# Performance work log

Measured on AMD Instinct MI355X. Metric: run time of the kernel, lower is better.

## Reference

```python
import jax, jax.numpy as jnp
import numpy as np

B, S, F = 32, 8, 4
N0, N1, N2 = 2048, 4096, 2048
H, OUT = 1024, 256
IN = N0 + N1 + N2  # 8192
SC_LAYERS = 2


def setup_inputs() -> dict:
    key = jax.random.key(0)
    ks = jax.random.split(key, 16)
    rn = jax.random.normal
    inp = {
        'xs0': rn(ks[0], (B, S, N0), jnp.float32),
        'xs1': rn(ks[1], (B, S, N1), jnp.float32),
        'xs2': rn(ks[2], (B, S, N2), jnp.float32),
        # dense Laplacians, scaled so L@x keeps unit-ish variance
        'L0': rn(ks[3], (N0, N0), jnp.float32) / np.sqrt(N0).astype(np.float32),
        'L1': rn(ks[4], (N1, N1), jnp.float32) / np.sqrt(N1).astype(np.float32),
        'L2': rn(ks[5], (N2, N2), jnp.float32) / np.sqrt(N2).astype(np.float32),
        # per-layer, per-filter diagonal weights (std=0.01 as in torch init)
        'Wc0': 0.01 * rn(ks[6], (SC_LAYERS, F, N0), jnp.float32),
        'Wc1': 0.01 * rn(ks[7], (SC_LAYERS, F, N1), jnp.float32),
        'Wc2': 0.01 * rn(ks[8], (SC_LAYERS, F, N2), jnp.float32),
        # MLP params (xavier-ish)
        'W_in': rn(ks[9], (IN, H), jnp.float32) / np.sqrt(IN).astype(np.float32),
        'b_in': jnp.zeros((H,), jnp.float32),
        'W_h': rn(ks[10], (H, H), jnp.float32) / np.sqrt(H).astype(np.float32),
        'b_h': jnp.zeros((H,), jnp.float32),
        'W_out': rn(ks[11], (H, OUT), jnp.float32) / np.sqrt(H).astype(np.float32),
        'b_out': jnp.zeros((OUT,), jnp.float32),
    }
    return inp


def _conv_stack(x, L, Wc):
    # x: [B, S, n]; L: [n, n]; Wc: [layers, F, n]
    for l in range(Wc.shape[0]):
        # batched Laplacian matmul: (L @ x_bs) for every (b, s)
        Lx = jnp.einsum('bsn,mn->bsm', x, L)  # [B, S, n]
        # diagonal filter scaling + activation + sum over filters (fused)
        x = jax.nn.relu(Lx[:, :, None, :] * Wc[l][None, None, :, :]).sum(axis=2)
    return x


def reference(xs0, xs1, xs2, L0, L1, L2, Wc0, Wc1, Wc2,
              W_in, b_in, W_h, b_h, W_out, b_out):
    h = jnp.concatenate([
        _conv_stack(xs0, L0, Wc0),
        _conv_stack(xs1, L1, Wc1),
        _conv_stack(xs2, L2, Wc2),
    ], axis=-1)                      # [B, S, IN]
    h = h.sum(axis=1)                # sum over sequence -> [B, IN]
    h = jax.nn.relu(h @ W_in + b_in)
    h = jax.nn.relu(h @ W_h + b_h)   # single hidden layer (nn_layers=2)
    return h @ W_out + b_out         # [B, OUT]
```

## Files before the change

kernel.cpp:

```cpp
#include <hip/hip_runtime.h>
#include <hip/hip_bf16.h>


#define B_    32
#define S_    8
#define BS_   256
#define F_    4
#define IN_   8192
#define H_    1024
#define OUT_  256

#define L_TOT  25165824LL
#define LOFF1  4194304LL
#define LOFF2  20971520LL

typedef __attribute__((ext_vector_type(8)))  short bf16x8;
typedef __attribute__((ext_vector_type(4)))  short short4v;
typedef __attribute__((ext_vector_type(8)))  short short8v;
typedef __attribute__((ext_vector_type(16))) float f32x16;

typedef const __attribute__((address_space(1))) void* gas_ptr;
typedef __attribute__((address_space(3))) void* las_ptr;

__device__ __forceinline__ void gload16(const void* g, void* s) {
    __builtin_amdgcn_global_load_lds((gas_ptr)g, (las_ptr)s, 16, 0, 0);
}

__device__ __forceinline__ unsigned short rne_bf16(float f) {
    unsigned int u = __builtin_bit_cast(unsigned int, f);
    u += 0x7FFFu + ((u >> 16) & 1u);
    return (unsigned short)(u >> 16);
}

__global__ void k_pre(const float* __restrict__ L0, const float* __restrict__ L1,
                      const float* __restrict__ L2, unsigned short* __restrict__ Lb,
                      const float* __restrict__ x0, const float* __restrict__ x1,
                      const float* __restrict__ x2,
                      unsigned short* __restrict__ Xhi, unsigned short* __restrict__ Xlo,
                      const float* __restrict__ Wc0, const float* __restrict__ Wc1,
                      const float* __restrict__ Wc2, float* __restrict__ PM)
{
    const int bx = blockIdx.x, tid = threadIdx.x;
    if (bx < 3072) {
        const long long base = (long long)bx * 8192 + tid * 8;
        #pragma unroll
        for (int u = 0; u < 4; ++u) {
            long long e = base + (long long)u * 2048;
            const float* src; long long off;
            if (e < LOFF1)      { src = L0; off = 0; }
            else if (e < LOFF2) { src = L1; off = LOFF1; }
            else                { src = L2; off = LOFF2; }
            const float* p = src + (e - off);
            float4 a = *(const float4*)(p);
            float4 b = *(const float4*)(p + 4);
            short8v o;
            o[0] = (short)rne_bf16(a.x); o[1] = (short)rne_bf16(a.y);
            o[2] = (short)rne_bf16(a.z); o[3] = (short)rne_bf16(a.w);
            o[4] = (short)rne_bf16(b.x); o[5] = (short)rne_bf16(b.y);
            o[6] = (short)rne_bf16(b.z); o[7] = (short)rne_bf16(b.w);
            *(short8v*)(Lb + e) = o;
        }
    } else if (bx < 3584) {
        const int base = (bx - 3072) * 4096 + tid * 8;
        #pragma unroll
        for (int u = 0; u < 2; ++u) {
            int e = base + u * 2048;
            int m = e >> 13, c = e & 8191;
            const float* src; int n, c0;
            if (c < 2048)      { src = x0; n = 2048; c0 = c; }
            else if (c < 6144) { src = x1; n = 4096; c0 = c - 2048; }
            else               { src = x2; n = 2048; c0 = c - 6144; }
            const float* p = src + (size_t)m * n + c0;
            float4 a = *(const float4*)(p);
            float4 b = *(const float4*)(p + 4);
            float v[8] = {a.x, a.y, a.z, a.w, b.x, b.y, b.z, b.w};
            short8v h, l;
            #pragma unroll
            for (int i = 0; i < 8; ++i) {
                unsigned short hb = rne_bf16(v[i]);
                float hf = __builtin_bit_cast(float, (unsigned int)hb << 16);
                h[i] = (short)hb;
                l[i] = (short)rne_bf16(v[i] - hf);
            }
            *(short8v*)(Xhi + (size_t)m * IN_ + c) = h;
            *(short8v*)(Xlo + (size_t)m * IN_ + c) = l;
        }
    } else {
        const int base = (bx - 3584) * 2048 + tid * 8;
        #pragma unroll
        for (int i = 0; i < 8; ++i) {
            int idx = base + i;
            int l = idx / IN_, n = idx % IN_;
            const float* Wc; int nb, j;
            if (n < 2048)      { Wc = Wc0; nb = 2048; j = n;        }
            else if (n < 6144) { Wc = Wc1; nb = 4096; j = n - 2048; }
            else               { Wc = Wc2; nb = 2048; j = n - 6144; }
            float p = 0.f, m = 0.f;
            #pragma unroll
            for (int f = 0; f < F_; ++f) {
                float w = Wc[(l * F_ + f) * nb + j];
                p += fmaxf(w, 0.f);
                m += fmaxf(-w, 0.f);
            }
            PM[(l * 2 + 0) * IN_ + n] = p;
            PM[(l * 2 + 1) * IN_ + n] = m;
        }
    }
}

__global__ __launch_bounds__(256, 3) void k_gemm(
    const unsigned short* __restrict__ Xhi, const unsigned short* __restrict__ Xlo,
    const unsigned short* __restrict__ Lb,
    float* __restrict__ pf)
{
    __shared__ __attribute__((aligned(16))) unsigned short Ah[3][64 * 32];
    __shared__ __attribute__((aligned(16))) unsigned short Al[3][64 * 32];
    __shared__ __attribute__((aligned(16))) unsigned short Bs[3][128 * 32];

    const int bx = blockIdx.x;
    int n_, noff, mt, nt, sk; long long loff;
    if (bx < 128) {
        int u = bx; sk = u & 1; u >>= 1; mt = u >> 4; nt = u & 15;
        n_ = 2048; noff = 0; loff = 0;
    } else if (bx < 640) {
        int u = bx - 128; sk = u & 3; u >>= 2; mt = u >> 5; nt = u & 31;
        n_ = 4096; noff = 2048; loff = LOFF1;
    } else {
        int u = bx - 640; sk = u & 1; u >>= 1; mt = u >> 4; nt = u & 15;
        n_ = 2048; noff = 6144; loff = LOFF2;
    }
    const int k0 = sk << 10;

    const int tid = threadIdx.x, l = tid & 63, w = tid >> 6;

    const int sr  = 16 * w + (l >> 2);
    const int slg = (((l & 3) ^ ((l >> 3) & 3)) << 3);
    const unsigned short* gAh = Xhi + (size_t)(mt * 64 + sr) * IN_ + noff + k0 + slg;
    const unsigned short* gAl = Xlo + (size_t)(mt * 64 + sr) * IN_ + noff + k0 + slg;
    const unsigned short* gB0 = Lb + loff + (size_t)(nt * 128 + sr) * n_ + k0 + slg;
    const unsigned short* gB1 = Lb + loff + (size_t)(nt * 128 + 64 + sr) * n_ + k0 + slg;

    const int l31 = l & 31, lh = l >> 5;
    const int wm = w >> 1, wn = w & 1;
    const int ra  = (wm * 32 + l31) * 32;
    const int rb0 = (wn * 64 + l31) * 32;
    const int rb1 = rb0 + 32 * 32;
    const int swz = ((l31 >> 1) & 3);

    f32x16 acc0, acc1;
    #pragma unroll
    for (int r = 0; r < 16; ++r) { acc0[r] = 0.f; acc1[r] = 0.f; }

    #define STAGE(slot, ko)                                                     \
        do {                                                                    \
            gload16(gAh + (ko), (char*)&Ah[slot][0] + w * 1024);                \
            gload16(gAl + (ko), (char*)&Al[slot][0] + w * 1024);                \
            gload16(gB0 + (ko), (char*)&Bs[slot][0] + w * 1024);                \
            gload16(gB1 + (ko), (char*)&Bs[slot][0] + 4096 + w * 1024);         \
        } while (0)

    STAGE(0, 0);
    STAGE(1, 32);

    for (int it = 0; it < 32; ++it) {
        if (it + 1 < 32) asm volatile("s_waitcnt vmcnt(4)" ::: "memory");
        else             asm volatile("s_waitcnt vmcnt(0)" ::: "memory");
        __builtin_amdgcn_s_barrier();
        asm volatile("" ::: "memory");

        if (it + 2 < 32) {
            const int slot = (it + 2) % 3;
            const int ko = (it + 2) * 32;
            STAGE(slot, ko);
        }
        __builtin_amdgcn_sched_barrier(0);

        const int cur = it % 3;
        #pragma unroll
        for (int t = 0; t < 2; ++t) {
            const int sidx = (((2 * t + lh) ^ swz) << 3);
            bf16x8 fah = *(const bf16x8*)&Ah[cur][ra + sidx];
            bf16x8 fal = *(const bf16x8*)&Al[cur][ra + sidx];
            bf16x8 fb0 = *(const bf16x8*)&Bs[cur][rb0 + sidx];
            bf16x8 fb1 = *(const bf16x8*)&Bs[cur][rb1 + sidx];
            acc0 = __builtin_amdgcn_mfma_f32_32x32x16_bf16(fal, fb0, acc0, 0, 0, 0);
            acc0 = __builtin_amdgcn_mfma_f32_32x32x16_bf16(fah, fb0, acc0, 0, 0, 0);
            acc1 = __builtin_amdgcn_mfma_f32_32x32x16_bf16(fal, fb1, acc1, 0, 0, 0);
            acc1 = __builtin_amdgcn_mfma_f32_32x32x16_bf16(fah, fb1, acc1, 0, 0, 0);
        }
        asm volatile("" ::: "memory");
    }
    #undef STAGE

    const int colg = noff + nt * 128 + wn * 64 + l31;
    float* po = pf + ((size_t)sk * 256 + (size_t)mt * 64 + wm * 32 + 4 * lh) * IN_;
    #pragma unroll
    for (int r = 0; r < 16; ++r) {
        int row = (r & 3) + 8 * (r >> 2);
        po[(size_t)row * IN_ + colg]      = acc0[r];
        po[(size_t)row * IN_ + colg + 32] = acc1[r];
    }
}

__global__ void k_epi0(const float* __restrict__ pf,
                       const float* __restrict__ Pv, const float* __restrict__ Mv,
                       unsigned short* __restrict__ Yhi, unsigned short* __restrict__ Ylo) {
    int e = (blockIdx.x * 256 + threadIdx.x) * 4;
    int m = e >> 13, c = e & 8191;
    const int nsl = (c >= 2048 && c < 6144) ? 4 : 2;
    const float* p0 = pf + (size_t)m * IN_ + c;
    float vs[4] = {0.f, 0.f, 0.f, 0.f};
    for (int s = 0; s < nsl; ++s) {
        float4 v = *(const float4*)(p0 + (size_t)s * 256 * IN_);
        vs[0] += v.x; vs[1] += v.y; vs[2] += v.z; vs[3] += v.w;
    }
    float4 pv = *(const float4*)(Pv + c);
    float4 mv = *(const float4*)(Mv + c);
    float pa[4] = {pv.x, pv.y, pv.z, pv.w};
    float ma[4] = {mv.x, mv.y, mv.z, mv.w};
    short hv[4], lv[4];
    #pragma unroll
    for (int j = 0; j < 4; ++j) {
        float y = fmaxf(vs[j], 0.f) * pa[j] + fmaxf(-vs[j], 0.f) * ma[j];
        unsigned short hb = rne_bf16(y);
        float hf = __builtin_bit_cast(float, (unsigned int)hb << 16);
        hv[j] = (short)hb;
        lv[j] = (short)rne_bf16(y - hf);
    }
    short4v h = {hv[0], hv[1], hv[2], hv[3]};
    short4v lo = {lv[0], lv[1], lv[2], lv[3]};
    *(short4v*)(Yhi + (size_t)m * IN_ + c) = h;
    *(short4v*)(Ylo + (size_t)m * IN_ + c) = lo;
}

__global__ void k_epi1s(const float* __restrict__ pf,
                        const float* __restrict__ Pv, const float* __restrict__ Mv,
                        float* __restrict__ hsum) {
    int e = (blockIdx.x * 256 + threadIdx.x) * 4;
    int b = e >> 13, c = e & 8191;
    const int nsl = (c >= 2048 && c < 6144) ? 4 : 2;
    float4 pv = *(const float4*)(Pv + c);
    float4 mv = *(const float4*)(Mv + c);
    float pa[4] = {pv.x, pv.y, pv.z, pv.w};
    float ma[4] = {mv.x, mv.y, mv.z, mv.w};
    float hs[4] = {0.f, 0.f, 0.f, 0.f};
    for (int q = 0; q < 8; ++q) {
        const int m = b * 8 + q;
        const float* p0 = pf + (size_t)m * IN_ + c;
        float vs[4] = {0.f, 0.f, 0.f, 0.f};
        for (int s = 0; s < nsl; ++s) {
            float4 v = *(const float4*)(p0 + (size_t)s * 256 * IN_);
            vs[0] += v.x; vs[1] += v.y; vs[2] += v.z; vs[3] += v.w;
        }
        #pragma unroll
        for (int j = 0; j < 4; ++j)
            hs[j] += fmaxf(vs[j], 0.f) * pa[j] + fmaxf(-vs[j], 0.f) * ma[j];
    }
    *(float4*)(hsum + (size_t)b * IN_ + c) = *(float4*)hs;
}

template<int KC>
__global__ __launch_bounds__(256) void k_mlp3(
    const float* __restrict__ X, const float* __restrict__ W,
    float* __restrict__ P, int K, int H)
{
    __shared__ float Xs[32][KC];
    const int tid = threadIdx.x;
    const int lane = tid & 63;
    const int mg = tid >> 6;
    const int h = (blockIdx.x * 64 + lane) * 4;
    const int c = blockIdx.y, k0 = c * KC;

    for (int i = tid * 4; i < 32 * KC; i += 1024) {
        int m = i / KC, kk = i % KC;
        *(float4*)&Xs[m][kk] = *(const float4*)(X + (size_t)m * K + k0 + kk);
    }
    __syncthreads();

    float4 acc[8];
    #pragma unroll
    for (int m = 0; m < 8; ++m) acc[m] = {0.f, 0.f, 0.f, 0.f};

    const float* wp = W + (size_t)k0 * H + h;
    for (int kk = 0; kk < KC; kk += 4) {
        float4 w4[4];
        #pragma unroll
        for (int u = 0; u < 4; ++u)
            w4[u] = *(const float4*)(wp + (size_t)(kk + u) * H);
        #pragma unroll
        for (int m = 0; m < 8; ++m) {
            float4 xv = *(const float4*)&Xs[mg * 8 + m][kk];
            acc[m].x = fmaf(xv.x, w4[0].x, acc[m].x);
            acc[m].y = fmaf(xv.x, w4[0].y, acc[m].y);
            acc[m].z = fmaf(xv.x, w4[0].z, acc[m].z);
            acc[m].w = fmaf(xv.x, w4[0].w, acc[m].w);
            acc[m].x = fmaf(xv.y, w4[1].x, acc[m].x);
            acc[m].y = fmaf(xv.y, w4[1].y, acc[m].y);
            acc[m].z = fmaf(xv.y, w4[1].z, acc[m].z);
            acc[m].w = fmaf(xv.y, w4[1].w, acc[m].w);
            acc[m].x = fmaf(xv.z, w4[2].x, acc[m].x);
            acc[m].y = fmaf(xv.z, w4[2].y, acc[m].y);
            acc[m].z = fmaf(xv.z, w4[2].z, acc[m].z);
            acc[m].w = fmaf(xv.z, w4[2].w, acc[m].w);
            acc[m].x = fmaf(xv.w, w4[3].x, acc[m].x);
            acc[m].y = fmaf(xv.w, w4[3].y, acc[m].y);
            acc[m].z = fmaf(xv.w, w4[3].z, acc[m].z);
            acc[m].w = fmaf(xv.w, w4[3].w, acc[m].w);
        }
    }
    #pragma unroll
    for (int m = 0; m < 8; ++m)
        *(float4*)(P + ((size_t)c * 32 + mg * 8 + m) * H + h) = acc[m];
}

__global__ void k_reduce4(const float* __restrict__ P, const float* __restrict__ bias,
                          float* __restrict__ Y, int NC, int MH4, int H, int do_relu) {
    int idx = blockIdx.x * 256 + threadIdx.x;
    if (idx >= MH4) return;
    int h0 = (idx * 4) % H;
    float4 s = *(const float4*)(bias + h0);
    for (int c = 0; c < NC; ++c) {
        float4 v = *(const float4*)(P + (size_t)c * MH4 * 4 + (size_t)idx * 4);
        s.x += v.x; s.y += v.y; s.z += v.z; s.w += v.w;
    }
    if (do_relu) {
        s.x = fmaxf(s.x, 0.f); s.y = fmaxf(s.y, 0.f);
        s.z = fmaxf(s.z, 0.f); s.w = fmaxf(s.w, 0.f);
    }
    *(float4*)(Y + (size_t)idx * 4) = s;
}

extern "C" void kernel_launch(void* const* d_in, const int* in_sizes, int n_in,
                              void* d_out, int out_size, void* d_ws, size_t ws_size,
                              hipStream_t stream) {
    const float* xs0  = (const float*)d_in[0];
    const float* xs1  = (const float*)d_in[1];
    const float* xs2  = (const float*)d_in[2];
    const float* L0   = (const float*)d_in[3];
    const float* L1   = (const float*)d_in[4];
    const float* L2   = (const float*)d_in[5];
    const float* Wc0  = (const float*)d_in[6];
    const float* Wc1  = (const float*)d_in[7];
    const float* Wc2  = (const float*)d_in[8];
    const float* W_in = (const float*)d_in[9];
    const float* b_in = (const float*)d_in[10];
    const float* W_h  = (const float*)d_in[11];
    const float* b_h  = (const float*)d_in[12];
    const float* W_out= (const float*)d_in[13];
    const float* b_out= (const float*)d_in[14];

    char* w = (char*)d_ws;
    float*          PM  = (float*)w;          w += (size_t)4 * IN_ * 4;
    unsigned short* Lb  = (unsigned short*)w; w += (size_t)L_TOT * 2;
    unsigned short* Xhi = (unsigned short*)w; w += (size_t)BS_ * IN_ * 2;
    unsigned short* Xlo = (unsigned short*)w; w += (size_t)BS_ * IN_ * 2;
    unsigned short* Yhi = (unsigned short*)w; w += (size_t)BS_ * IN_ * 2;
    unsigned short* Ylo = (unsigned short*)w; w += (size_t)BS_ * IN_ * 2;
    float*          pf  = (float*)w;          w += (size_t)4 * BS_ * IN_ * 4;
    float*          hsum= (float*)w;          w += (size_t)32 * IN_ * 4;
    float*          p1  = pf;
    float*          h1  = (float*)w;          w += (size_t)32 * H_ * 4;
    float*          p2  = (float*)w;          w += (size_t)32 * 32 * H_ * 4;
    float*          h2  = (float*)w;          w += (size_t)32 * H_ * 4;
    float*          p3  = (float*)w;          w += (size_t)32 * 32 * OUT_ * 4;

    k_pre<<<3592, 256, 0, stream>>>(L0, L1, L2, Lb, xs0, xs1, xs2, Xhi, Xlo,
                                    Wc0, Wc1, Wc2, PM);

    k_gemm<<<768, 256, 0, stream>>>(Xhi, Xlo, Lb, pf);
    k_epi0<<<2048, 256, 0, stream>>>(pf, PM + 0 * IN_, PM + 1 * IN_, Yhi, Ylo);
    k_gemm<<<768, 256, 0, stream>>>(Yhi, Ylo, Lb, pf);
    k_epi1s<<<256, 256, 0, stream>>>(pf, PM + 2 * IN_, PM + 3 * IN_, hsum);

    {
        dim3 g(4, 128);
        k_mlp3<64><<<g, 256, 0, stream>>>(hsum, W_in, p1, IN_, H_);
        k_reduce4<<<32, 256, 0, stream>>>(p1, b_in, h1, 128, 8192, H_, 1);
    }
    {
        dim3 g(4, 32);
        k_mlp3<32><<<g, 256, 0, stream>>>(h1, W_h, p2, H_, H_);
        k_reduce4<<<32, 256, 0, stream>>>(p2, b_h, h2, 32, 8192, H_, 1);
    }
    {
        dim3 g(1, 32);
        k_mlp3<32><<<g, 256, 0, stream>>>(h2, W_out, p3, H_, OUT_);
        k_reduce4<<<8, 256, 0, stream>>>(p3, b_out, (float*)d_out, 32, 2048, OUT_, 0);
    }
}
```

Baseline: 199.2 us.

## Enlarge GEMM block tile to 128x256 with XCD-aware block mapping

The Laplacian GEMM now has each block compute a 128x256 output tile instead of 64x128. Each wave holds 2x4 MFMA accumulators, and the grid shrinks from 768 to 192 blocks. Block indices are remapped so the two M-tiles sharing one L tile land on the same XCD, which should improve L2 reuse of the bf16 Laplacian. The aim is more MFMA work per LDS load and less global traffic per FLOP. The trade-off is heavier register and LDS use per block: occupancy drops to one block per CU and 192 blocks only partly fill the device's CUs.

```diff
diff --git a/kernel.cpp b/kernel.cpp
--- a/kernel.cpp
+++ b/kernel.cpp
@@ -108,97 +108,120 @@
     }
 }
 
-__global__ __launch_bounds__(256, 3) void k_gemm(
+__global__ __launch_bounds__(256, 1) void k_gemm(
     const unsigned short* __restrict__ Xhi, const unsigned short* __restrict__ Xlo,
     const unsigned short* __restrict__ Lb,
     float* __restrict__ pf)
 {
-    __shared__ __attribute__((aligned(16))) unsigned short Ah[3][64 * 32];
-    __shared__ __attribute__((aligned(16))) unsigned short Al[3][64 * 32];
-    __shared__ __attribute__((aligned(16))) unsigned short Bs[3][128 * 32];
+    __shared__ __attribute__((aligned(16))) unsigned short Ah[3][128 * 32];
+    __shared__ __attribute__((aligned(16))) unsigned short Al[3][128 * 32];
+    __shared__ __attribute__((aligned(16))) unsigned short Bs[3][256 * 32];
 
     const int bx = blockIdx.x;
-    int n_, noff, mt, nt, sk; long long loff;
-    if (bx < 128) {
-        int u = bx; sk = u & 1; u >>= 1; mt = u >> 4; nt = u & 15;
-        n_ = 2048; noff = 0; loff = 0;
-    } else if (bx < 640) {
-        int u = bx - 128; sk = u & 3; u >>= 2; mt = u >> 5; nt = u & 31;
-        n_ = 4096; noff = 2048; loff = LOFF1;
-    } else {
-        int u = bx - 640; sk = u & 1; u >>= 1; mt = u >> 4; nt = u & 15;
-        n_ = 2048; noff = 6144; loff = LOFF2;
-    }
+    const int xcd = bx & 7, rr = bx >> 3;
+    const int mt = rr & 1;
+    const int j = xcd * 12 + (rr >> 1);
+    int n_, noff, nt, sk; long long loff;
+    if (j < 16)      { sk = j & 1;          nt = j >> 1;  n_ = 2048; noff = 0;    loff = 0;     }
+    else if (j < 80) { int u = j - 16; sk = u & 3; nt = u >> 2; n_ = 4096; noff = 2048; loff = LOFF1; }
+    else             { int u = j - 80; sk = u & 1; nt = u >> 1; n_ = 2048; noff = 6144; loff = LOFF2; }
     const int k0 = sk << 10;
 
-    const int tid = threadIdx.x, l = tid & 63, w = tid >> 6;
-
-    const int sr  = 16 * w + (l >> 2);
-    const int slg = (((l & 3) ^ ((l >> 3) & 3)) << 3);
-    const unsigned short* gAh = Xhi + (size_t)(mt * 64 + sr) * IN_ + noff + k0 + slg;
-    const unsigned short* gAl = Xlo + (size_t)(mt * 64 + sr) * IN_ + noff + k0 + slg;
-    const unsigned short* gB0 = Lb + loff + (size_t)(nt * 128 + sr) * n_ + k0 + slg;
-    const unsigned short* gB1 = Lb + loff + (size_t)(nt * 128 + 64 + sr) * n_ + k0 + slg;
-
+    const int tid = threadIdx.x;
+
+    const int srow = tid >> 2;
+    const int scol = (((tid & 3) ^ ((tid >> 3) & 3)) << 3);
+    const unsigned short* gAh = Xhi + (size_t)(mt * 128 + srow) * IN_ + noff + k0 + scol;
+    const unsigned short* gAl = Xlo + (size_t)(mt * 128 + srow) * IN_ + noff + k0 + scol;
+    const unsigned short* gB  = Lb + loff + (size_t)(nt * 256 + srow) * n_ + k0 + scol;
+    const size_t aq = (size_t)64 * IN_;
+    const size_t bq = (size_t)64 * n_;
+    const int tb = tid * 16;
+
+    char *aC = (char*)&Ah[0][0], *aN = (char*)&Ah[1][0], *aS = (char*)&Ah[2][0];
+    char *lC = (char*)&Al[0][0], *lN = (char*)&Al[1][0], *lS = (char*)&Al[2][0];
+    char *bC = (char*)&Bs[0][0], *bN = (char*)&Bs[1][0], *bS = (char*)&Bs[2][0];
+
+    #define STAGE(pA, pL, pB, ko)                                           \
+        do {                                                                \
+            gload16(gAh + (ko),      pA + tb);                              \
+            gload16(gAh + (ko) + aq, pA + 4096 + tb);                       \
+            gload16(gAl + (ko),      pL + tb);                              \
+            gload16(gAl + (ko) + aq, pL + 4096 + tb);                       \
+            gload16(gB + (ko),           pB + tb);                          \
+            gload16(gB + (ko) + bq,      pB + 4096 + tb);                   \
+            gload16(gB + (ko) + 2 * bq,  pB + 8192 + tb);                   \
+            gload16(gB + (ko) + 3 * bq,  pB + 12288 + tb);                  \
+        } while (0)
+
+    const int l = tid & 63, w = tid >> 6;
     const int l31 = l & 31, lh = l >> 5;
     const int wm = w >> 1, wn = w & 1;
-    const int ra  = (wm * 32 + l31) * 32;
-    const int rb0 = (wn * 64 + l31) * 32;
-    const int rb1 = rb0 + 32 * 32;
-    const int swz = ((l31 >> 1) & 3);
-
-    f32x16 acc0, acc1;
+    const int swzl = (l31 >> 1) & 3;
+    const int arow = (wm * 64 + l31) * 32;
+    const int brow = (wn * 128 + l31) * 32;
+
+    f32x16 acc[2][4];
     #pragma unroll
-    for (int r = 0; r < 16; ++r) { acc0[r] = 0.f; acc1[r] = 0.f; }
-
-    #define STAGE(slot, ko)                                                     \
-        do {                                                                    \
-            gload16(gAh + (ko), (char*)&Ah[slot][0] + w * 1024);                \
-            gload16(gAl + (ko), (char*)&Al[slot][0] + w * 1024);                \
-            gload16(gB0 + (ko), (char*)&Bs[slot][0] + w * 1024);                \
-            gload16(gB1 + (ko), (char*)&Bs[slot][0] + 4096 + w * 1024);         \
-        } while (0)
-
-    STAGE(0, 0);
-    STAGE(1, 32);
+    for (int r = 0; r < 2; ++r)
+        #pragma unroll
+        for (int c = 0; c < 4; ++c)
+            #pragma unroll
+            for (int e = 0; e < 16; ++e) acc[r][c][e] = 0.f;
+
+    STAGE(aC, lC, bC, 0);
+    STAGE(aN, lN, bN, 32);
 
     for (int it = 0; it < 32; ++it) {
-        if (it + 1 < 32) asm volatile("s_waitcnt vmcnt(4)" ::: "memory");
-        else             asm volatile("s_waitcnt vmcnt(0)" ::: "memory");
+        if (it < 31) asm volatile("s_waitcnt vmcnt(8)" ::: "memory");
+        else         asm volatile("s_waitcnt vmcnt(0)" ::: "memory");
         __builtin_amdgcn_s_barrier();
         asm volatile("" ::: "memory");
 
-        if (it + 2 < 32) {
-            const int slot = (it + 2) % 3;
-            const int ko = (it + 2) * 32;
-            STAGE(slot, ko);
-        }
-        __builtin_amdgcn_sched_barrier(0);
-
-        const int cur = it % 3;
+        if (it + 2 < 32) STAGE(aS, lS, bS, (it + 2) * 32);
+
+        const unsigned short* cA = (const unsigned short*)aC;
+        const unsigned short* cL = (const unsigned short*)lC;
+        const unsigned short* cB = (const unsigned short*)bC;
         #pragma unroll
         for (int t = 0; t < 2; ++t) {
-            const int sidx = (((2 * t + lh) ^ swz) << 3);
-            bf16x8 fah = *(const bf16x8*)&Ah[cur][ra + sidx];
-            bf16x8 fal = *(const bf16x8*)&Al[cur][ra + sidx];
-            bf16x8 fb0 = *(const bf16x8*)&Bs[cur][rb0 + sidx];
-            bf16x8 fb1 = *(const bf16x8*)&Bs[cur][rb1 + sidx];
-            acc0 = __builtin_amdgcn_mfma_f32_32x32x16_bf16(fal, fb0, acc0, 0, 0, 0);
-            acc0 = __builtin_amdgcn_mfma_f32_32x32x16_bf16(fah, fb0, acc0, 0, 0, 0);
-            acc1 = __builtin_amdgcn_mfma_f32_32x32x16_bf16(fal, fb1, acc1, 0, 0, 0);
-            acc1 = __builtin_amdgcn_mfma_f32_32x32x16_bf16(fah, fb1, acc1, 0, 0, 0);
+            const int sidx = (((t << 1) + lh) ^ swzl) << 3;
+            bf16x8 fah[2], fal[2], fb[4];
+            #pragma unroll
+            for (int r = 0; r < 2; ++r) {
+                fah[r] = *(const bf16x8*)&cA[arow + r * 1024 + sidx];
+                fal[r] = *(const bf16x8*)&cL[arow + r * 1024 + sidx];
+            }
+            #pragma unroll
+            for (int c = 0; c < 4; ++c)
+                fb[c] = *(const bf16x8*)&cB[brow + c * 1024 + sidx];
+            #pragma unroll
+            for (int r = 0; r < 2; ++r)
+                #pragma unroll
+                for (int c = 0; c < 4; ++c) {
+                    acc[r][c] = __builtin_amdgcn_mfma_f32_32x32x16_bf16(fal[r], fb[c], acc[r][c], 0, 0, 0);
+                    acc[r][c] = __builtin_amdgcn_mfma_f32_32x32x16_bf16(fah[r], fb[c], acc[r][c], 0, 0, 0);
+                }
         }
         asm volatile("" ::: "memory");
+
+        char* t1 = aC; aC = aN; aN = aS; aS = t1;
+        char* t2 = lC; lC = lN; lN = lS; lS = t2;
+        char* t3 = bC; bC = bN; bN = bS; bS = t3;
     }
     #undef STAGE
 
-    const int colg = noff + nt * 128 + wn * 64 + l31;
-    float* po = pf + ((size_t)sk * 256 + (size_t)mt * 64 + wm * 32 + 4 * lh) * IN_;
+    const int colg = noff + nt * 256 + wn * 128 + l31;
     #pragma unroll
-    for (int r = 0; r < 16; ++r) {
-        int row = (r & 3) + 8 * (r >> 2);
-        po[(size_t)row * IN_ + colg]      = acc0[r];
-        po[(size_t)row * IN_ + colg + 32] = acc1[r];
+    for (int r = 0; r < 2; ++r) {
+        float* po = pf + ((size_t)sk * 256 + mt * 128 + wm * 64 + r * 32 + 4 * lh) * IN_;
+        #pragma unroll
+        for (int e = 0; e < 16; ++e) {
+            const int row = (e & 3) + 8 * (e >> 2);
+            #pragma unroll
+            for (int c = 0; c < 4; ++c)
+                po[(size_t)row * IN_ + colg + c * 32] = acc[r][c][e];
+        }
     }
 }
 
@@ -367,9 +390,9 @@
     k_pre<<<3592, 256, 0, stream>>>(L0, L1, L2, Lb, xs0, xs1, xs2, Xhi, Xlo,
                                     Wc0, Wc1, Wc2, PM);
 
-    k_gemm<<<768, 256, 0, stream>>>(Xhi, Xlo, Lb, pf);
+    k_gemm<<<192, 256, 0, stream>>>(Xhi, Xlo, Lb, pf);
     k_epi0<<<2048, 256, 0, stream>>>(pf, PM + 0 * IN_, PM + 1 * IN_, Yhi, Ylo);
-    k_gemm<<<768, 256, 0, stream>>>(Yhi, Ylo, Lb, pf);
+    k_gemm<<<192, 256, 0, stream>>>(Yhi, Ylo, Lb, pf);
     k_epi1s<<<256, 256, 0, stream>>>(pf, PM + 2 * IN_, PM + 3 * IN_, hsum);
 
     {
```

Measured after the change: 225.3 us. 1.13x slower.

## Load A fragments directly to registers, keep LDS staging only for B

Applied to the files above, without the earlier changes.

The GEMM no longer stages the X hi/lo tiles through shared memory. Each lane loads its A fragments from global memory straight into registers, one iteration ahead, while only the Laplacian B tile goes through the three-slot LDS ring, which is now rotated with pointer swaps. The waitcnt values are adjusted to the new count of outstanding loads. The preprocessing kernel also hoists the L source selection out of its loop per block and issues all of its loads before any conversion. This cuts LDS traffic and footprint, but adds register pressure and makes the A reads less coalesced, since wave lanes are spread across rows.

```diff
diff --git a/kernel.cpp b/kernel.cpp
--- a/kernel.cpp
+++ b/kernel.cpp
@@ -42,23 +42,26 @@
 {
     const int bx = blockIdx.x, tid = threadIdx.x;
     if (bx < 3072) {
-        const long long base = (long long)bx * 8192 + tid * 8;
-        #pragma unroll
-        for (int u = 0; u < 4; ++u) {
-            long long e = base + (long long)u * 2048;
-            const float* src; long long off;
-            if (e < LOFF1)      { src = L0; off = 0; }
-            else if (e < LOFF2) { src = L1; off = LOFF1; }
-            else                { src = L2; off = LOFF2; }
-            const float* p = src + (e - off);
-            float4 a = *(const float4*)(p);
-            float4 b = *(const float4*)(p + 4);
+        const long long b0 = (long long)bx * 8192;
+        const float* src; long long off;
+        if (b0 < LOFF1)      { src = L0; off = 0; }
+        else if (b0 < LOFF2) { src = L1; off = LOFF1; }
+        else                 { src = L2; off = LOFF2; }
+        const float* p2 = src + (b0 - off) + tid * 8;
+        float4 va[4], vb[4];
+        #pragma unroll
+        for (int j = 0; j < 4; ++j) {
+            va[j] = *(const float4*)(p2 + j * 2048);
+            vb[j] = *(const float4*)(p2 + j * 2048 + 4);
+        }
+        #pragma unroll
+        for (int j = 0; j < 4; ++j) {
             short8v o;
-            o[0] = (short)rne_bf16(a.x); o[1] = (short)rne_bf16(a.y);
-            o[2] = (short)rne_bf16(a.z); o[3] = (short)rne_bf16(a.w);
-            o[4] = (short)rne_bf16(b.x); o[5] = (short)rne_bf16(b.y);
-            o[6] = (short)rne_bf16(b.z); o[7] = (short)rne_bf16(b.w);
-            *(short8v*)(Lb + e) = o;
+            o[0] = (short)rne_bf16(va[j].x); o[1] = (short)rne_bf16(va[j].y);
+            o[2] = (short)rne_bf16(va[j].z); o[3] = (short)rne_bf16(va[j].w);
+            o[4] = (short)rne_bf16(vb[j].x); o[5] = (short)rne_bf16(vb[j].y);
+            o[6] = (short)rne_bf16(vb[j].z); o[7] = (short)rne_bf16(vb[j].w);
+            *(short8v*)(Lb + b0 + j * 2048 + tid * 8) = o;
         }
     } else if (bx < 3584) {
         const int base = (bx - 3072) * 4096 + tid * 8;
@@ -113,8 +116,6 @@
     const unsigned short* __restrict__ Lb,
     float* __restrict__ pf)
 {
-    __shared__ __attribute__((aligned(16))) unsigned short Ah[3][64 * 32];
-    __shared__ __attribute__((aligned(16))) unsigned short Al[3][64 * 32];
     __shared__ __attribute__((aligned(16))) unsigned short Bs[3][128 * 32];
 
     const int bx = blockIdx.x;
@@ -133,64 +134,76 @@
 
     const int tid = threadIdx.x, l = tid & 63, w = tid >> 6;
 
-    const int sr  = 16 * w + (l >> 2);
-    const int slg = (((l & 3) ^ ((l >> 3) & 3)) << 3);
-    const unsigned short* gAh = Xhi + (size_t)(mt * 64 + sr) * IN_ + noff + k0 + slg;
-    const unsigned short* gAl = Xlo + (size_t)(mt * 64 + sr) * IN_ + noff + k0 + slg;
-    const unsigned short* gB0 = Lb + loff + (size_t)(nt * 128 + sr) * n_ + k0 + slg;
-    const unsigned short* gB1 = Lb + loff + (size_t)(nt * 128 + 64 + sr) * n_ + k0 + slg;
+    const int sg = ((tid & 3) ^ ((tid >> 3) & 3)) << 3;
+    const unsigned short* gB0 = Lb + loff + (size_t)(nt * 128 + (tid >> 2)) * n_ + k0 + sg;
+    const unsigned short* gB1 = gB0 + (size_t)64 * n_;
+    const int tb = tid * 16;
+
+    char *bC = (char*)&Bs[0][0], *bN = (char*)&Bs[1][0], *bS = (char*)&Bs[2][0];
+
+    #define STAGE_B(dst, ko)                                   \
+        do {                                                   \
+            gload16(gB0 + (ko), (dst) + tb);                   \
+            gload16(gB1 + (ko), (dst) + 4096 + tb);            \
+        } while (0)
 
     const int l31 = l & 31, lh = l >> 5;
     const int wm = w >> 1, wn = w & 1;
-    const int ra  = (wm * 32 + l31) * 32;
+    const unsigned short* pAh = Xhi + (size_t)(mt * 64 + wm * 32 + l31) * IN_ + noff + k0 + lh * 8;
+    const unsigned short* pAl = Xlo + (size_t)(mt * 64 + wm * 32 + l31) * IN_ + noff + k0 + lh * 8;
+
+    const int swz = (l31 >> 1) & 3;
     const int rb0 = (wn * 64 + l31) * 32;
     const int rb1 = rb0 + 32 * 32;
-    const int swz = ((l31 >> 1) & 3);
 
     f32x16 acc0, acc1;
     #pragma unroll
     for (int r = 0; r < 16; ++r) { acc0[r] = 0.f; acc1[r] = 0.f; }
 
-    #define STAGE(slot, ko)                                                     \
-        do {                                                                    \
-            gload16(gAh + (ko), (char*)&Ah[slot][0] + w * 1024);                \
-            gload16(gAl + (ko), (char*)&Al[slot][0] + w * 1024);                \
-            gload16(gB0 + (ko), (char*)&Bs[slot][0] + w * 1024);                \
-            gload16(gB1 + (ko), (char*)&Bs[slot][0] + 4096 + w * 1024);         \
-        } while (0)
-
-    STAGE(0, 0);
-    STAGE(1, 32);
+    STAGE_B(bC, 0);
+    STAGE_B(bN, 32);
+    bf16x8 aCh0 = *(const bf16x8*)(pAh);
+    bf16x8 aCh1 = *(const bf16x8*)(pAh + 16);
+    bf16x8 aCl0 = *(const bf16x8*)(pAl);
+    bf16x8 aCl1 = *(const bf16x8*)(pAl + 16);
 
     for (int it = 0; it < 32; ++it) {
-        if (it + 1 < 32) asm volatile("s_waitcnt vmcnt(4)" ::: "memory");
-        else             asm volatile("s_waitcnt vmcnt(0)" ::: "memory");
+        bf16x8 aNh0, aNh1, aNl0, aNl1;
+        if (it + 1 < 32) {
+            const int ko = (it + 1) * 32;
+            aNh0 = *(const bf16x8*)(pAh + ko);
+            aNh1 = *(const bf16x8*)(pAh + ko + 16);
+            aNl0 = *(const bf16x8*)(pAl + ko);
+            aNl1 = *(const bf16x8*)(pAl + ko + 16);
+        }
+
+        if (it == 0)       asm volatile("s_waitcnt vmcnt(4)" ::: "memory");
+        else if (it == 31) asm volatile("s_waitcnt vmcnt(0)" ::: "memory");
+        else               asm volatile("s_waitcnt vmcnt(6)" ::: "memory");
         __builtin_amdgcn_s_barrier();
         asm volatile("" ::: "memory");
 
-        if (it + 2 < 32) {
-            const int slot = (it + 2) % 3;
-            const int ko = (it + 2) * 32;
-            STAGE(slot, ko);
-        }
-        __builtin_amdgcn_sched_barrier(0);
-
-        const int cur = it % 3;
+        if (it + 2 < 32) STAGE_B(bS, (it + 2) * 32);
+
+        const unsigned short* cB = (const unsigned short*)bC;
         #pragma unroll
         for (int t = 0; t < 2; ++t) {
-            const int sidx = (((2 * t + lh) ^ swz) << 3);
-            bf16x8 fah = *(const bf16x8*)&Ah[cur][ra + sidx];
-            bf16x8 fal = *(const bf16x8*)&Al[cur][ra + sidx];
-            bf16x8 fb0 = *(const bf16x8*)&Bs[cur][rb0 + sidx];
-            bf16x8 fb1 = *(const bf16x8*)&Bs[cur][rb1 + sidx];
+            const int sidx = (((t << 1) + lh) ^ swz) << 3;
+            bf16x8 fb0 = *(const bf16x8*)&cB[rb0 + sidx];
+            bf16x8 fb1 = *(const bf16x8*)&cB[rb1 + sidx];
+            bf16x8 fah = t ? aCh1 : aCh0;
+            bf16x8 fal = t ? aCl1 : aCl0;
             acc0 = __builtin_amdgcn_mfma_f32_32x32x16_bf16(fal, fb0, acc0, 0, 0, 0);
             acc0 = __builtin_amdgcn_mfma_f32_32x32x16_bf16(fah, fb0, acc0, 0, 0, 0);
             acc1 = __builtin_amdgcn_mfma_f32_32x32x16_bf16(fal, fb1, acc1, 0, 0, 0);
             acc1 = __builtin_amdgcn_mfma_f32_32x32x16_bf16(fah, fb1, acc1, 0, 0, 0);
         }
         asm volatile("" ::: "memory");
-    }
-    #undef STAGE
+
+        if (it + 1 < 32) { aCh0 = aNh0; aCh1 = aNh1; aCl0 = aNl0; aCl1 = aNl1; }
+        char* tmp = bC; bC = bN; bN = bS; bS = tmp;
+    }
+    #undef STAGE_B
 
     const int colg = noff + nt * 128 + wn * 64 + l31;
     float* po = pf + ((size_t)sk * 256 + (size_t)mt * 64 + wm * 32 + 4 * lh) * IN_;
```

Measured after the change: 254.6 us. +27.8%, slower.
